# Optimization experiments

Hardware: AMD Instinct MI355X
Metric: run time of the kernel (lower is better)

Reference implementation:

```python
import jax, jax.numpy as jnp
import numpy as np

N_HEAD = 12

def setup_inputs() -> dict:
    key = jax.random.key(0)
    k1, k2, k3, k4, k5 = jax.random.split(key, 5)
    B, T, C = 16, 1024, 768
    s = 0.02
    return {
        "x": jax.random.normal(k1, (B, T, C), dtype=jnp.float32),
        "W_attn": jax.random.normal(k2, (C, 3 * C), dtype=jnp.float32) * s,
        "b_attn": jax.random.normal(k3, (3 * C,), dtype=jnp.float32) * s,
        "W_proj": jax.random.normal(k4, (C, C), dtype=jnp.float32) * s,
        "b_proj": jax.random.normal(k5, (C,), dtype=jnp.float32) * s,
    }

def reference(x, W_attn, b_attn, W_proj, b_proj):
    B, T, C = x.shape
    H = N_HEAD
    d = C // H
    qkv = x @ W_attn + b_attn                      # [B,T,3C]
    q, k, v = jnp.split(qkv, 3, axis=-1)
    # [B,H,T,d]
    q = q.reshape(B, T, H, d).transpose(0, 2, 1, 3)
    k = k.reshape(B, T, H, d).transpose(0, 2, 1, 3)
    v = v.reshape(B, T, H, d).transpose(0, 2, 1, 3)
    scale = 1.0 / jnp.sqrt(jnp.array(d, dtype=x.dtype))
    att = jnp.einsum('bhqd,bhkd->bhqk', q, k) * scale   # [B,H,T,T]
    causal = jnp.tril(jnp.ones((T, T), dtype=bool))
    att = jnp.where(causal[None, None], att, -jnp.inf)
    att = jax.nn.softmax(att, axis=-1)
    # dropout is identity in eval mode (p=0 for deterministic reference)
    y = jnp.einsum('bhqk,bhkd->bhqd', att, v)            # [B,H,T,d]
    y = y.transpose(0, 2, 1, 3).reshape(B, T, C)
    return y @ W_proj + b_proj
```

## Files before the change

### kernel.cpp

```cpp
#include <hip/hip_runtime.h>
#include <cstddef>


typedef __bf16 bf16_t;
typedef __bf16 bf16x4 __attribute__((ext_vector_type(4)));
typedef __bf16 bf16x8 __attribute__((ext_vector_type(8)));
typedef float  f32x4  __attribute__((ext_vector_type(4)));

#define MFMA16(a,b,c) __builtin_amdgcn_mfma_f32_16x16x32_bf16((a),(b),(c),0,0,0)
#define GLOAD16(gp, lp) \
  __builtin_amdgcn_global_load_lds((const __attribute__((address_space(1))) unsigned int*)(gp), \
                                   (__attribute__((address_space(3))) unsigned int*)(lp), 16, 0, 0)

#define SWZ(row, c) (((row) * 64) + ((((c) ^ ((row) & 7)) * 8)))

#define QSCALE 0.1803368801111f

__global__ __launch_bounds__(256)
void xcast_kernel(const float* __restrict__ in, bf16_t* __restrict__ out)
{
    const size_t i = ((size_t)blockIdx.x * 256 + threadIdx.x) * 4;
    float4 f = *(const float4*)(in + i);
    bf16x4 o = {(bf16_t)f.x, (bf16_t)f.y, (bf16_t)f.z, (bf16_t)f.w};
    *(bf16x4*)(out + i) = o;
}

__global__ __launch_bounds__(256)
void tcast_kernel(const float* __restrict__ in, bf16_t* __restrict__ out, int R, int Cn)
{
    __shared__ bf16_t tile[32][33];
    const int tx = threadIdx.x & 31, ty = threadIdx.x >> 5;
    const int c0 = blockIdx.x * 32, r0 = blockIdx.y * 32;
#pragma unroll
    for (int i = 0; i < 4; ++i)
        tile[ty + i*8][tx] = (bf16_t)in[(size_t)(r0 + ty + i*8) * Cn + c0 + tx];
    __syncthreads();
#pragma unroll
    for (int i = 0; i < 4; ++i)
        out[(size_t)(c0 + ty + i*8) * R + r0 + tx] = tile[tx][ty + i*8];
}

__global__ __launch_bounds__(256)
void qkv_gemm(const bf16_t* __restrict__ Xb, const bf16_t* __restrict__ WT,
              const float* __restrict__ bias,
              bf16_t* __restrict__ Qb, bf16_t* __restrict__ Kb, bf16_t* __restrict__ VT)
{
    __shared__ bf16_t As[128 * 64];
    __shared__ bf16_t Bs[128 * 64];
    const int tid = threadIdx.x;
    const int w = tid >> 6, l = tid & 63;
    const int lm = l & 15, lq = l >> 4;
    const int wy = w >> 1, wx = w & 1;
    const int lr = l >> 3;
    const int lcs = ((l & 7) ^ lr) * 8;
    const int nt = blockIdx.x * 128, mt = blockIdx.y * 128;

    f32x4 acc[4][4];
    const f32x4 z4 = {0.f, 0.f, 0.f, 0.f};
#pragma unroll
    for (int i = 0; i < 4; ++i)
#pragma unroll
        for (int j = 0; j < 4; ++j) acc[i][j] = z4;

    for (int kt = 0; kt < 768; kt += 64) {
#pragma unroll
        for (int p = 0; p < 4; ++p) {
            const int row = w * 32 + p * 8;
            GLOAD16(Xb + (size_t)(mt + row + lr) * 768 + kt + lcs, &As[row * 64]);
            GLOAD16(WT + (size_t)(nt + row + lr) * 768 + kt + lcs, &Bs[row * 64]);
        }
        __syncthreads();
#pragma unroll
        for (int ks = 0; ks < 2; ++ks) {
            const int c = ks * 4 + lq;
            bf16x8 aw[4], bx[4];
#pragma unroll
            for (int i = 0; i < 4; ++i)
                aw[i] = *(const bf16x8*)(&Bs[SWZ(wx * 64 + i * 16 + lm, c)]);
#pragma unroll
            for (int j = 0; j < 4; ++j)
                bx[j] = *(const bf16x8*)(&As[SWZ(wy * 64 + j * 16 + lm, c)]);
#pragma unroll
            for (int i = 0; i < 4; ++i)
#pragma unroll
                for (int j = 0; j < 4; ++j)
                    acc[i][j] = MFMA16(aw[i], bx[j], acc[i][j]);
        }
        __syncthreads();
    }

    const int nb = nt + wx * 64;
    const int which = nb / 768;
    const int h = (nb % 768) >> 6;
    const int b_ = mt >> 10;
    const int tbase = (mt & 1023) + wy * 64;
    if (which == 2) {
        bf16_t* vt = VT + (size_t)(b_ * 12 + h) * 65536;
#pragma unroll
        for (int i = 0; i < 4; ++i) {
            const float4 bv = *(const float4*)(bias + nb + i * 16 + lq * 4);
            const int d0 = i * 16 + lq * 4;
#pragma unroll
            for (int j = 0; j < 4; ++j) {
                const int t = tbase + j * 16 + lm;
                f32x4 v = acc[i][j];
                vt[(size_t)(d0 + 0) * 1024 + t] = (bf16_t)(v[0] + bv.x);
                vt[(size_t)(d0 + 1) * 1024 + t] = (bf16_t)(v[1] + bv.y);
                vt[(size_t)(d0 + 2) * 1024 + t] = (bf16_t)(v[2] + bv.z);
                vt[(size_t)(d0 + 3) * 1024 + t] = (bf16_t)(v[3] + bv.w);
            }
        }
    } else {
        bf16_t* dst = (which == 0) ? Qb : Kb;
        const float qs = (which == 0) ? QSCALE : 1.0f;
#pragma unroll
        for (int i = 0; i < 4; ++i) {
            const float4 bv = *(const float4*)(bias + nb + i * 16 + lq * 4);
            const int d0 = i * 16 + lq * 4;
#pragma unroll
            for (int j = 0; j < 4; ++j) {
                const int t = tbase + j * 16 + lm;
                f32x4 v = acc[i][j];
                bf16x4 o4 = {(bf16_t)((v[0] + bv.x) * qs), (bf16_t)((v[1] + bv.y) * qs),
                             (bf16_t)((v[2] + bv.z) * qs), (bf16_t)((v[3] + bv.w) * qs)};
                *(bf16x4*)(dst + ((size_t)(b_ * 12 + h) * 1024 + t) * 64 + d0) = o4;
            }
        }
    }
}

__global__ __launch_bounds__(256, 3)
void attn_kernel(const bf16_t* __restrict__ Qb, const bf16_t* __restrict__ Kb,
                 const bf16_t* __restrict__ VT, bf16_t* __restrict__ Y)
{
    __shared__ bf16_t Ks[2][64 * 64];
    __shared__ bf16_t Vs[2][64 * 64];
    __shared__ bf16_t Plds[4 * 16 * 72];
    const int tid = threadIdx.x;
    const int w = tid >> 6, l = tid & 63;
    const int lm = l & 15, lq = l >> 4;
    const int lr = l >> 3;
    const int lc8 = ((l & 7) ^ lr) * 8;
    const int xp = blockIdx.x;
    const int bh = blockIdx.y;
    const int loq = xp * 128, hiq = (7 - xp) * 128;

    int qmin[4];
    qmin[0] = loq + w * 32;      qmin[1] = qmin[0] + 16;
    qmin[2] = hiq + w * 32;      qmin[3] = qmin[2] + 16;

    const bf16_t* Kbase = Kb + (size_t)bh * 65536;
    const bf16_t* Vbase = VT + (size_t)bh * 65536;
    bf16_t* Pw = &Plds[w * 1152];
    const int r0a = w * 16, r0b = w * 16 + 8;

    bf16x8 bq[4][2];
#pragma unroll
    for (int m = 0; m < 4; ++m) {
        const bf16_t* Qp = Qb + ((size_t)bh * 1024 + qmin[m] + lm) * 64;
        bq[m][0] = *(const bf16x8*)(Qp + lq * 8);
        bq[m][1] = *(const bf16x8*)(Qp + 32 + lq * 8);
    }

    f32x4 O[4][4];
    float li[4] = {0.f, 0.f, 0.f, 0.f};
    const f32x4 z4 = {0.f, 0.f, 0.f, 0.f};
#pragma unroll
    for (int m = 0; m < 4; ++m)
#pragma unroll
        for (int s = 0; s < 4; ++s) O[m][s] = z4;

    const int kend = hiq + 64;

    GLOAD16(Kbase + (size_t)(r0a + lr) * 64 + lc8,   &Ks[0][r0a * 64]);
    GLOAD16(Kbase + (size_t)(r0b + lr) * 64 + lc8,   &Ks[0][r0b * 64]);
    GLOAD16(Vbase + (size_t)(r0a + lr) * 1024 + lc8, &Vs[0][r0a * 64]);
    GLOAD16(Vbase + (size_t)(r0b + lr) * 1024 + lc8, &Vs[0][r0b * 64]);
    __syncthreads();

    int cb = 0;
    for (int k0 = 0; k0 <= kend; k0 += 64) {
        const int nxt = cb ^ 1;
        if (k0 + 64 <= kend) {
            const int kn = k0 + 64;
            if (nxt) {
                GLOAD16(Kbase + (size_t)(kn + r0a + lr) * 64 + lc8,        &Ks[1][r0a * 64]);
                GLOAD16(Kbase + (size_t)(kn + r0b + lr) * 64 + lc8,        &Ks[1][r0b * 64]);
                GLOAD16(Vbase + (size_t)(r0a + lr) * 1024 + kn + lc8,      &Vs[1][r0a * 64]);
                GLOAD16(Vbase + (size_t)(r0b + lr) * 1024 + kn + lc8,      &Vs[1][r0b * 64]);
            } else {
                GLOAD16(Kbase + (size_t)(kn + r0a + lr) * 64 + lc8,        &Ks[0][r0a * 64]);
                GLOAD16(Kbase + (size_t)(kn + r0b + lr) * 64 + lc8,        &Ks[0][r0b * 64]);
                GLOAD16(Vbase + (size_t)(r0a + lr) * 1024 + kn + lc8,      &Vs[0][r0a * 64]);
                GLOAD16(Vbase + (size_t)(r0b + lr) * 1024 + kn + lc8,      &Vs[0][r0b * 64]);
            }
        }
        const bf16_t* Kc = Ks[cb];
        const bf16_t* Vc = Vs[cb];
#pragma unroll
        for (int m = 0; m < 4; ++m) {
            if (k0 > qmin[m] + 15) continue;
            f32x4 S[4];
#pragma unroll
            for (int s = 0; s < 4; ++s) S[s] = z4;
#pragma unroll
            for (int ks = 0; ks < 2; ++ks)
#pragma unroll
                for (int s = 0; s < 4; ++s) {
                    bf16x8 ak = *(const bf16x8*)(&Kc[SWZ(s * 16 + lm, ks * 4 + lq)]);
                    S[s] = MFMA16(ak, bq[m][ks], S[s]);
                }
            if (k0 + 63 > qmin[m]) {
                const int q = qmin[m] + lm;
#pragma unroll
                for (int s = 0; s < 4; ++s)
#pragma unroll
                    for (int rg = 0; rg < 4; ++rg)
                        if (k0 + s * 16 + lq * 4 + rg > q) S[s][rg] = -1e30f;
            }
            float ls = 0.f;
#pragma unroll
            for (int s = 0; s < 4; ++s)
#pragma unroll
                for (int rg = 0; rg < 4; ++rg) {
                    float pv = exp2f(S[s][rg]);
                    S[s][rg] = pv;
                    ls += pv;
                }
            li[m] += ls;
#pragma unroll
            for (int s = 0; s < 4; ++s) {
                bf16x4 p4 = {(bf16_t)S[s][0], (bf16_t)S[s][1],
                             (bf16_t)S[s][2], (bf16_t)S[s][3]};
                *(bf16x4*)(&Pw[lm * 72 + s * 16 + lq * 4]) = p4;
            }
#pragma unroll
            for (int ks = 0; ks < 2; ++ks) {
                bf16x8 bp = *(const bf16x8*)(&Pw[lm * 72 + ks * 32 + lq * 8]);
#pragma unroll
                for (int s = 0; s < 4; ++s) {
                    bf16x8 av = *(const bf16x8*)(&Vc[SWZ(s * 16 + lm, ks * 4 + lq)]);
                    O[m][s] = MFMA16(av, bp, O[m][s]);
                }
            }
        }
        __syncthreads();
        cb = nxt;
    }

    const int b = bh / 12, h = bh % 12;
#pragma unroll
    for (int m = 0; m < 4; ++m) {
        float s0 = li[m];
        s0 += __shfl_xor(s0, 16, 64);
        s0 += __shfl_xor(s0, 32, 64);
        const float inv = 1.f / s0;
        const size_t row = ((size_t)(b * 1024 + qmin[m] + lm)) * 768 + h * 64;
#pragma unroll
        for (int s = 0; s < 4; ++s) {
            bf16x4 y4 = {(bf16_t)(O[m][s][0] * inv), (bf16_t)(O[m][s][1] * inv),
                         (bf16_t)(O[m][s][2] * inv), (bf16_t)(O[m][s][3] * inv)};
            *(bf16x4*)(Y + row + s * 16 + lq * 4) = y4;
        }
    }
}

__global__ __launch_bounds__(256)
void proj_gemm(const bf16_t* __restrict__ A, const bf16_t* __restrict__ WT,
               const float* __restrict__ bias, float* __restrict__ out)
{
    __shared__ bf16_t As[128 * 64];
    __shared__ bf16_t Bs[128 * 64];
    const int tid = threadIdx.x;
    const int w = tid >> 6, l = tid & 63;
    const int lm = l & 15, lq = l >> 4;
    const int wy = w >> 1, wx = w & 1;
    const int lr = l >> 3;
    const int lcs = ((l & 7) ^ lr) * 8;
    const int nt = blockIdx.x * 128, mt = blockIdx.y * 128;

    f32x4 acc[4][4];
    const f32x4 z4 = {0.f, 0.f, 0.f, 0.f};
#pragma unroll
    for (int i = 0; i < 4; ++i)
#pragma unroll
        for (int j = 0; j < 4; ++j) acc[i][j] = z4;

    for (int kt = 0; kt < 768; kt += 64) {
#pragma unroll
        for (int p = 0; p < 4; ++p) {
            const int row = w * 32 + p * 8;
            GLOAD16(A  + (size_t)(mt + row + lr) * 768 + kt + lcs, &As[row * 64]);
            GLOAD16(WT + (size_t)(nt + row + lr) * 768 + kt + lcs, &Bs[row * 64]);
        }
        __syncthreads();
#pragma unroll
        for (int ks = 0; ks < 2; ++ks) {
            const int c = ks * 4 + lq;
            bf16x8 aw[4], bx[4];
#pragma unroll
            for (int i = 0; i < 4; ++i)
                aw[i] = *(const bf16x8*)(&Bs[SWZ(wx * 64 + i * 16 + lm, c)]);
#pragma unroll
            for (int j = 0; j < 4; ++j)
                bx[j] = *(const bf16x8*)(&As[SWZ(wy * 64 + j * 16 + lm, c)]);
#pragma unroll
            for (int i = 0; i < 4; ++i)
#pragma unroll
                for (int j = 0; j < 4; ++j)
                    acc[i][j] = MFMA16(aw[i], bx[j], acc[i][j]);
        }
        __syncthreads();
    }
#pragma unroll
    for (int i = 0; i < 4; ++i) {
        const int n0 = nt + wx * 64 + i * 16 + lq * 4;
        const float4 bv = *(const float4*)(bias + n0);
#pragma unroll
        for (int j = 0; j < 4; ++j) {
            const int t = mt + wy * 64 + j * 16 + lm;
            f32x4 v = acc[i][j];
            float4 o = {v[0] + bv.x, v[1] + bv.y, v[2] + bv.z, v[3] + bv.w};
            *(float4*)(out + (size_t)t * 768 + n0) = o;
        }
    }
}

extern "C" void kernel_launch(void* const* d_in, const int* in_sizes, int n_in,
                              void* d_out, int out_size, void* d_ws, size_t ws_size,
                              hipStream_t stream)
{
    const float* x      = (const float*)d_in[0];
    const float* W_attn = (const float*)d_in[1];
    const float* b_attn = (const float*)d_in[2];
    const float* W_proj = (const float*)d_in[3];
    const float* b_proj = (const float*)d_in[4];
    float* out = (float*)d_out;

    char* ws = (char*)d_ws;
    const size_t SZ = (size_t)16 * 12 * 1024 * 64 * 2;
    bf16_t* Qb  = (bf16_t*)(ws);
    bf16_t* Kb  = (bf16_t*)(ws + SZ);
    bf16_t* VT  = (bf16_t*)(ws + 3 * SZ);
    bf16_t* Yb  = (bf16_t*)(ws + 4 * SZ);
    bf16_t* Xb  = (bf16_t*)(ws + 4 * SZ);
    bf16_t* WaT = (bf16_t*)(ws + 5 * SZ);
    bf16_t* WpT = (bf16_t*)(ws + 5 * SZ + (size_t)2304 * 768 * 2);

    xcast_kernel<<<12288, 256, 0, stream>>>(x, Xb);
    tcast_kernel<<<dim3(72, 24), 256, 0, stream>>>(W_attn, WaT, 768, 2304);
    tcast_kernel<<<dim3(24, 24), 256, 0, stream>>>(W_proj, WpT, 768, 768);
    qkv_gemm<<<dim3(18, 128), 256, 0, stream>>>(Xb, WaT, b_attn, Qb, Kb, VT);
    attn_kernel<<<dim3(4, 192), 256, 0, stream>>>(Qb, Kb, VT, Yb);
    proj_gemm<<<dim3(6, 128), 256, 0, stream>>>(Yb, WpT, b_proj, out);
}
```

Baseline: 290.6 us.

## Rewrite QKV GEMM as 256x256 8-wave double-buffered pipelined kernel

Replaces the 128x128, 4-wave QKV GEMM with a 256x256 tile, 8-wave kernel. It double-buffers LDS, interleaves global-to-LDS staging with MFMA phases under explicit barriers and wait counts, raises wave priority around MFMAs, and remaps blocks to XCDs. The aim is to hide load latency and raise data reuse per tile. In exchange it uses far more registers and LDS (128KB) and depends on hand-written synchronization, which lowers occupancy.

```diff
diff --git a/kernel.cpp b/kernel.cpp
--- a/kernel.cpp
+++ b/kernel.cpp
@@ -40,70 +40,161 @@
         out[(size_t)(c0 + ty + i*8) * R + r0 + tx] = tile[tx][ty + i*8];
 }
 
-__global__ __launch_bounds__(256)
-void qkv_gemm(const bf16_t* __restrict__ Xb, const bf16_t* __restrict__ WT,
-              const float* __restrict__ bias,
-              bf16_t* __restrict__ Qb, bf16_t* __restrict__ Kb, bf16_t* __restrict__ VT)
-{
-    __shared__ bf16_t As[128 * 64];
-    __shared__ bf16_t Bs[128 * 64];
+#define LGKM0() asm volatile("s_waitcnt lgkmcnt(0)" ::: "memory")
+#define VMC(n)  asm volatile("s_waitcnt vmcnt(" #n ")" ::: "memory")
+#define PBAR()  __builtin_amdgcn_s_barrier()
+#define PRIO1() __builtin_amdgcn_s_setprio(1)
+#define PRIO0() __builtin_amdgcn_s_setprio(0)
+
+#define STAGE_HT(buf, kt, ht) do { \
+    const int r0_ = w * 16 + (((ht) & 1) ? 128 : 0); \
+    if ((ht) < 2) { \
+        GLOAD16(WT + (size_t)(nt + r0_ + lr) * 768 + (kt) + lcs,     &Bs[buf][r0_ * 64]); \
+        GLOAD16(WT + (size_t)(nt + r0_ + 8 + lr) * 768 + (kt) + lcs, &Bs[buf][(r0_ + 8) * 64]); \
+    } else { \
+        GLOAD16(Xb + (size_t)(mt + r0_ + lr) * 768 + (kt) + lcs,     &As[buf][r0_ * 64]); \
+        GLOAD16(Xb + (size_t)(mt + r0_ + 8 + lr) * 768 + (kt) + lcs, &As[buf][(r0_ + 8) * 64]); \
+    } \
+} while (0)
+
+#define RD_BX(dst, buf) do { \
+    _Pragma("unroll") for (int j_ = 0; j_ < 4; ++j_) \
+    _Pragma("unroll") for (int ks_ = 0; ks_ < 2; ++ks_) \
+        (dst)[j_][ks_] = *(const bf16x8*)(&As[buf][SWZ(wc * 64 + j_ * 16 + lm, ks_ * 4 + lq)]); \
+} while (0)
+
+#define RD_AW(dst, buf, F0, NF) do { \
+    _Pragma("unroll") for (int p_ = 0; p_ < (NF); ++p_) \
+    _Pragma("unroll") for (int ks_ = 0; ks_ < 2; ++ks_) \
+        (dst)[p_][ks_] = *(const bf16x8*)(&Bs[buf][SWZ(wr * 128 + ((F0) + p_) * 16 + lm, ks_ * 4 + lq)]); \
+} while (0)
+
+#define MFMA_Q(AW, BX, F0) do { \
+    _Pragma("unroll") for (int ks_ = 0; ks_ < 2; ++ks_) \
+    _Pragma("unroll") for (int p_ = 0; p_ < 2; ++p_) \
+    _Pragma("unroll") for (int j_ = 0; j_ < 4; ++j_) \
+        acc[(F0) + p_][j_] = MFMA16((AW)[p_][ks_], (BX)[j_][ks_], acc[(F0) + p_][j_]); \
+} while (0)
+
+__global__ __launch_bounds__(512)
+void qkv_gemm8(const bf16_t* __restrict__ Xb, const bf16_t* __restrict__ WT,
+               const float* __restrict__ bias,
+               bf16_t* __restrict__ Qb, bf16_t* __restrict__ Kb, bf16_t* __restrict__ VT)
+{
+    __shared__ bf16_t As[2][256 * 64];
+    __shared__ bf16_t Bs[2][256 * 64];
     const int tid = threadIdx.x;
     const int w = tid >> 6, l = tid & 63;
     const int lm = l & 15, lq = l >> 4;
-    const int wy = w >> 1, wx = w & 1;
     const int lr = l >> 3;
     const int lcs = ((l & 7) ^ lr) * 8;
-    const int nt = blockIdx.x * 128, mt = blockIdx.y * 128;
-
-    f32x4 acc[4][4];
+    const int wr = w >> 2, wc = w & 3;
+
+    const int g = blockIdx.x;
+    const int gt = (g & 7) * 72 + (g >> 3);
+    const int bm = gt / 9, bn = gt % 9;
+    const int mt = bm * 256, nt = bn * 256;
+
+    f32x4 acc[8][4];
     const f32x4 z4 = {0.f, 0.f, 0.f, 0.f};
 #pragma unroll
-    for (int i = 0; i < 4; ++i)
+    for (int i = 0; i < 8; ++i)
 #pragma unroll
         for (int j = 0; j < 4; ++j) acc[i][j] = z4;
 
-    for (int kt = 0; kt < 768; kt += 64) {
-#pragma unroll
-        for (int p = 0; p < 4; ++p) {
-            const int row = w * 32 + p * 8;
-            GLOAD16(Xb + (size_t)(mt + row + lr) * 768 + kt + lcs, &As[row * 64]);
-            GLOAD16(WT + (size_t)(nt + row + lr) * 768 + kt + lcs, &Bs[row * 64]);
-        }
-        __syncthreads();
-#pragma unroll
-        for (int ks = 0; ks < 2; ++ks) {
-            const int c = ks * 4 + lq;
-            bf16x8 aw[4], bx[4];
-#pragma unroll
-            for (int i = 0; i < 4; ++i)
-                aw[i] = *(const bf16x8*)(&Bs[SWZ(wx * 64 + i * 16 + lm, c)]);
-#pragma unroll
-            for (int j = 0; j < 4; ++j)
-                bx[j] = *(const bf16x8*)(&As[SWZ(wy * 64 + j * 16 + lm, c)]);
-#pragma unroll
-            for (int i = 0; i < 4; ++i)
-#pragma unroll
-                for (int j = 0; j < 4; ++j)
-                    acc[i][j] = MFMA16(aw[i], bx[j], acc[i][j]);
-        }
-        __syncthreads();
-    }
-
-    const int nb = nt + wx * 64;
-    const int which = nb / 768;
-    const int h = (nb % 768) >> 6;
+    bf16x8 bx0[4][2], bx1[4][2];
+    bf16x8 aw0[2][2], aw12[4][2], aw3[2][2];
+
+    STAGE_HT(0, 0, 0); STAGE_HT(0, 0, 1); STAGE_HT(0, 0, 2); STAGE_HT(0, 0, 3);
+    STAGE_HT(1, 64, 0); STAGE_HT(1, 64, 1);
+    VMC(4);
+    PBAR();
+    RD_BX(bx0, 0); RD_AW(aw0, 0, 0, 2);
+
+#pragma unroll 1
+    for (int it = 0; it < 5; ++it) {
+        const int kv = it * 128 + 64, ku2 = kv + 64, kv2 = ku2 + 64;
+        RD_AW(aw12, 0, 2, 4);
+        STAGE_HT(1, kv, 2);
+        PBAR(); LGKM0();
+        PRIO1(); MFMA_Q(aw0, bx0, 0); PRIO0();
+        PBAR();
+        RD_AW(aw3, 0, 6, 2);
+        STAGE_HT(1, kv, 3);
+        PBAR(); LGKM0();
+        PRIO1(); MFMA_Q(aw12, bx0, 2); PRIO0();
+        PBAR();
+        STAGE_HT(0, ku2, 0);
+        PBAR();
+        PRIO1(); MFMA_Q(&aw12[2], bx0, 4); PRIO0();
+        VMC(2);
+        PBAR();
+        RD_BX(bx1, 1); RD_AW(aw0, 1, 0, 2);
+        STAGE_HT(0, ku2, 1);
+        PBAR(); LGKM0();
+        PRIO1(); MFMA_Q(aw3, bx0, 6); PRIO0();
+        PBAR();
+        RD_AW(aw12, 1, 2, 4);
+        STAGE_HT(0, ku2, 2);
+        PBAR(); LGKM0();
+        PRIO1(); MFMA_Q(aw0, bx1, 0); PRIO0();
+        PBAR();
+        RD_AW(aw3, 1, 6, 2);
+        STAGE_HT(0, ku2, 3);
+        PBAR(); LGKM0();
+        PRIO1(); MFMA_Q(aw12, bx1, 2); PRIO0();
+        PBAR();
+        STAGE_HT(1, kv2, 0);
+        PBAR();
+        PRIO1(); MFMA_Q(&aw12[2], bx1, 4); PRIO0();
+        VMC(2);
+        PBAR();
+        RD_BX(bx0, 0); RD_AW(aw0, 0, 0, 2);
+        STAGE_HT(1, kv2, 1);
+        PBAR(); LGKM0();
+        PRIO1(); MFMA_Q(aw3, bx1, 6); PRIO0();
+        PBAR();
+    }
+
+    RD_AW(aw12, 0, 2, 4);
+    STAGE_HT(1, 704, 2);
+    PBAR(); LGKM0();
+    PRIO1(); MFMA_Q(aw0, bx0, 0); PRIO0();
+    PBAR();
+    RD_AW(aw3, 0, 6, 2);
+    STAGE_HT(1, 704, 3);
+    PBAR(); LGKM0();
+    PRIO1(); MFMA_Q(aw12, bx0, 2); PRIO0();
+    PBAR();
+    PRIO1(); MFMA_Q(&aw12[2], bx0, 4); PRIO0();
+    VMC(0);
+    PBAR();
+    RD_BX(bx1, 1); RD_AW(aw0, 1, 0, 2);
+    MFMA_Q(aw3, bx0, 6);
+    RD_AW(aw12, 1, 2, 4);
+    LGKM0();
+    MFMA_Q(aw0, bx1, 0);
+    MFMA_Q(aw12, bx1, 2);
+    RD_AW(aw3, 1, 6, 2);
+    LGKM0();
+    MFMA_Q(&aw12[2], bx1, 4);
+    MFMA_Q(aw3, bx1, 6);
+
+    const int which = (nt) / 768;
     const int b_ = mt >> 10;
-    const int tbase = (mt & 1023) + wy * 64;
+    const int tb = (mt & 1023) + wc * 64;
     if (which == 2) {
-        bf16_t* vt = VT + (size_t)(b_ * 12 + h) * 65536;
-#pragma unroll
-        for (int i = 0; i < 4; ++i) {
-            const float4 bv = *(const float4*)(bias + nb + i * 16 + lq * 4);
-            const int d0 = i * 16 + lq * 4;
+#pragma unroll
+        for (int f = 0; f < 8; ++f) {
+            const int nglob = nt + wr * 128 + f * 16 + lq * 4;
+            const int nin = nglob - 1536;
+            const int h = nin >> 6, d0 = nin & 63;
+            bf16_t* vt = VT + (size_t)(b_ * 12 + h) * 65536;
+            const float4 bv = *(const float4*)(bias + nglob);
 #pragma unroll
             for (int j = 0; j < 4; ++j) {
-                const int t = tbase + j * 16 + lm;
-                f32x4 v = acc[i][j];
+                const int t = tb + j * 16 + lm;
+                f32x4 v = acc[f][j];
                 vt[(size_t)(d0 + 0) * 1024 + t] = (bf16_t)(v[0] + bv.x);
                 vt[(size_t)(d0 + 1) * 1024 + t] = (bf16_t)(v[1] + bv.y);
                 vt[(size_t)(d0 + 2) * 1024 + t] = (bf16_t)(v[2] + bv.z);
@@ -114,13 +205,15 @@
         bf16_t* dst = (which == 0) ? Qb : Kb;
         const float qs = (which == 0) ? QSCALE : 1.0f;
 #pragma unroll
-        for (int i = 0; i < 4; ++i) {
-            const float4 bv = *(const float4*)(bias + nb + i * 16 + lq * 4);
-            const int d0 = i * 16 + lq * 4;
+        for (int f = 0; f < 8; ++f) {
+            const int nglob = nt + wr * 128 + f * 16 + lq * 4;
+            const int nin = nglob - which * 768;
+            const int h = nin >> 6, d0 = nin & 63;
+            const float4 bv = *(const float4*)(bias + nglob);
 #pragma unroll
             for (int j = 0; j < 4; ++j) {
-                const int t = tbase + j * 16 + lm;
-                f32x4 v = acc[i][j];
+                const int t = tb + j * 16 + lm;
+                f32x4 v = acc[f][j];
                 bf16x4 o4 = {(bf16_t)((v[0] + bv.x) * qs), (bf16_t)((v[1] + bv.y) * qs),
                              (bf16_t)((v[2] + bv.z) * qs), (bf16_t)((v[3] + bv.w) * qs)};
                 *(bf16x4*)(dst + ((size_t)(b_ * 12 + h) * 1024 + t) * 64 + d0) = o4;
@@ -350,7 +443,7 @@
     xcast_kernel<<<12288, 256, 0, stream>>>(x, Xb);
     tcast_kernel<<<dim3(72, 24), 256, 0, stream>>>(W_attn, WaT, 768, 2304);
     tcast_kernel<<<dim3(24, 24), 256, 0, stream>>>(W_proj, WpT, 768, 768);
-    qkv_gemm<<<dim3(18, 128), 256, 0, stream>>>(Xb, WaT, b_attn, Qb, Kb, VT);
+    qkv_gemm8<<<576, 512, 0, stream>>>(Xb, WaT, b_attn, Qb, Kb, VT);
     attn_kernel<<<dim3(4, 192), 256, 0, stream>>>(Qb, Kb, VT, Yb);
     proj_gemm<<<dim3(6, 128), 256, 0, stream>>>(Yb, WpT, b_proj, out);
 }
```

Result: no change. 291.6 us (+0.3%).

## Enlarge QKV GEMM tile to 256x256 with 512 threads and block swizzle

Applied to the files above, without the earlier changes.

The QKV projection GEMM now uses 256x256 output tiles computed by 8 waves, each holding an 8x4 grid of MFMA accumulators. The grid is flattened to 576 blocks with a remapping that groups blocks for better L2 reuse. The next K slice is issued right after the post-compute barrier, but shared memory is still single-buffered, so loads and compute do not truly overlap. The goal is higher arithmetic intensity per byte loaded, at the cost of 64KB of LDS, more registers per thread and fewer resident blocks.

```diff
diff --git a/kernel.cpp b/kernel.cpp
--- a/kernel.cpp
+++ b/kernel.cpp
@@ -40,70 +40,84 @@
         out[(size_t)(c0 + ty + i*8) * R + r0 + tx] = tile[tx][ty + i*8];
 }
 
-__global__ __launch_bounds__(256)
+__global__ __launch_bounds__(512)
 void qkv_gemm(const bf16_t* __restrict__ Xb, const bf16_t* __restrict__ WT,
               const float* __restrict__ bias,
               bf16_t* __restrict__ Qb, bf16_t* __restrict__ Kb, bf16_t* __restrict__ VT)
 {
-    __shared__ bf16_t As[128 * 64];
-    __shared__ bf16_t Bs[128 * 64];
+    __shared__ bf16_t As[256 * 64];
+    __shared__ bf16_t Bs[256 * 64];
     const int tid = threadIdx.x;
     const int w = tid >> 6, l = tid & 63;
     const int lm = l & 15, lq = l >> 4;
-    const int wy = w >> 1, wx = w & 1;
     const int lr = l >> 3;
     const int lcs = ((l & 7) ^ lr) * 8;
-    const int nt = blockIdx.x * 128, mt = blockIdx.y * 128;
-
-    f32x4 acc[4][4];
+    const int wr = w >> 2, wc = w & 3;
+
+    const int g = blockIdx.x;
+    const int gt = (g & 7) * 72 + (g >> 3);
+    const int bm = gt / 9, bn = gt % 9;
+    const int mt = bm * 256, nt = bn * 256;
+
+    f32x4 acc[8][4];
     const f32x4 z4 = {0.f, 0.f, 0.f, 0.f};
 #pragma unroll
-    for (int i = 0; i < 4; ++i)
+    for (int i = 0; i < 8; ++i)
 #pragma unroll
         for (int j = 0; j < 4; ++j) acc[i][j] = z4;
 
+#define STAGE_ALL(kt) do { \
+    _Pragma("unroll") for (int ht_ = 0; ht_ < 4; ++ht_) { \
+        const int r0_ = w * 16 + ((ht_ & 1) ? 128 : 0); \
+        if (ht_ < 2) { \
+            GLOAD16(WT + (size_t)(nt + r0_ + lr) * 768 + (kt) + lcs,     &Bs[r0_ * 64]); \
+            GLOAD16(WT + (size_t)(nt + r0_ + 8 + lr) * 768 + (kt) + lcs, &Bs[(r0_ + 8) * 64]); \
+        } else { \
+            GLOAD16(Xb + (size_t)(mt + r0_ + lr) * 768 + (kt) + lcs,     &As[r0_ * 64]); \
+            GLOAD16(Xb + (size_t)(mt + r0_ + 8 + lr) * 768 + (kt) + lcs, &As[(r0_ + 8) * 64]); \
+        } \
+    } \
+} while (0)
+
+    STAGE_ALL(0);
     for (int kt = 0; kt < 768; kt += 64) {
-#pragma unroll
-        for (int p = 0; p < 4; ++p) {
-            const int row = w * 32 + p * 8;
-            GLOAD16(Xb + (size_t)(mt + row + lr) * 768 + kt + lcs, &As[row * 64]);
-            GLOAD16(WT + (size_t)(nt + row + lr) * 768 + kt + lcs, &Bs[row * 64]);
-        }
         __syncthreads();
 #pragma unroll
         for (int ks = 0; ks < 2; ++ks) {
-            const int c = ks * 4 + lq;
-            bf16x8 aw[4], bx[4];
-#pragma unroll
-            for (int i = 0; i < 4; ++i)
-                aw[i] = *(const bf16x8*)(&Bs[SWZ(wx * 64 + i * 16 + lm, c)]);
+            bf16x8 aw[8], bx[4];
+#pragma unroll
+            for (int p = 0; p < 8; ++p)
+                aw[p] = *(const bf16x8*)(&Bs[SWZ(wr * 128 + p * 16 + lm, ks * 4 + lq)]);
 #pragma unroll
             for (int j = 0; j < 4; ++j)
-                bx[j] = *(const bf16x8*)(&As[SWZ(wy * 64 + j * 16 + lm, c)]);
-#pragma unroll
-            for (int i = 0; i < 4; ++i)
+                bx[j] = *(const bf16x8*)(&As[SWZ(wc * 64 + j * 16 + lm, ks * 4 + lq)]);
+#pragma unroll
+            for (int p = 0; p < 8; ++p)
 #pragma unroll
                 for (int j = 0; j < 4; ++j)
-                    acc[i][j] = MFMA16(aw[i], bx[j], acc[i][j]);
-        }
-        __syncthreads();
-    }
-
-    const int nb = nt + wx * 64;
-    const int which = nb / 768;
-    const int h = (nb % 768) >> 6;
+                    acc[p][j] = MFMA16(aw[p], bx[j], acc[p][j]);
+        }
+        if (kt < 704) {
+            __syncthreads();
+            STAGE_ALL(kt + 64);
+        }
+    }
+
+    const int which = (nt) / 768;
     const int b_ = mt >> 10;
-    const int tbase = (mt & 1023) + wy * 64;
+    const int tb = (mt & 1023) + wc * 64;
     if (which == 2) {
-        bf16_t* vt = VT + (size_t)(b_ * 12 + h) * 65536;
-#pragma unroll
-        for (int i = 0; i < 4; ++i) {
-            const float4 bv = *(const float4*)(bias + nb + i * 16 + lq * 4);
-            const int d0 = i * 16 + lq * 4;
+#pragma unroll
+        for (int f = 0; f < 8; ++f) {
+            const int nglob = nt + wr * 128 + f * 16 + lq * 4;
+            const int nin = nglob - 1536;
+            const int h = nin >> 6, d0 = nin & 63;
+            bf16_t* vt = VT + (size_t)(b_ * 12 + h) * 65536;
+            const float4 bv = *(const float4*)(bias + nglob);
 #pragma unroll
             for (int j = 0; j < 4; ++j) {
-                const int t = tbase + j * 16 + lm;
-                f32x4 v = acc[i][j];
+                const int t = tb + j * 16 + lm;
+                f32x4 v = acc[f][j];
                 vt[(size_t)(d0 + 0) * 1024 + t] = (bf16_t)(v[0] + bv.x);
                 vt[(size_t)(d0 + 1) * 1024 + t] = (bf16_t)(v[1] + bv.y);
                 vt[(size_t)(d0 + 2) * 1024 + t] = (bf16_t)(v[2] + bv.z);
@@ -114,19 +128,22 @@
         bf16_t* dst = (which == 0) ? Qb : Kb;
         const float qs = (which == 0) ? QSCALE : 1.0f;
 #pragma unroll
-        for (int i = 0; i < 4; ++i) {
-            const float4 bv = *(const float4*)(bias + nb + i * 16 + lq * 4);
-            const int d0 = i * 16 + lq * 4;
+        for (int f = 0; f < 8; ++f) {
+            const int nglob = nt + wr * 128 + f * 16 + lq * 4;
+            const int nin = nglob - which * 768;
+            const int h = nin >> 6, d0 = nin & 63;
+            const float4 bv = *(const float4*)(bias + nglob);
 #pragma unroll
             for (int j = 0; j < 4; ++j) {
-                const int t = tbase + j * 16 + lm;
-                f32x4 v = acc[i][j];
+                const int t = tb + j * 16 + lm;
+                f32x4 v = acc[f][j];
                 bf16x4 o4 = {(bf16_t)((v[0] + bv.x) * qs), (bf16_t)((v[1] + bv.y) * qs),
                              (bf16_t)((v[2] + bv.z) * qs), (bf16_t)((v[3] + bv.w) * qs)};
                 *(bf16x4*)(dst + ((size_t)(b_ * 12 + h) * 1024 + t) * 64 + d0) = o4;
             }
         }
     }
+#undef STAGE_ALL
 }
 
 __global__ __launch_bounds__(256, 3)
@@ -350,7 +367,7 @@
     xcast_kernel<<<12288, 256, 0, stream>>>(x, Xb);
     tcast_kernel<<<dim3(72, 24), 256, 0, stream>>>(W_attn, WaT, 768, 2304);
     tcast_kernel<<<dim3(24, 24), 256, 0, stream>>>(W_proj, WpT, 768, 768);
-    qkv_gemm<<<dim3(18, 128), 256, 0, stream>>>(Xb, WaT, b_attn, Qb, Kb, VT);
+    qkv_gemm<<<576, 512, 0, stream>>>(Xb, WaT, b_attn, Qb, Kb, VT);
     attn_kernel<<<dim3(4, 192), 256, 0, stream>>>(Qb, Kb, VT, Yb);
     proj_gemm<<<dim3(6, 128), 256, 0, stream>>>(Yb, WpT, b_proj, out);
 }
```

Result: no change. 292.8 us (+0.8%).
